# Kernel optimization log

Measured on AMD Instinct MI355X. Metric: run time of the kernel, lower is better.

The kernel has to match this reference:

```python
import jax, jax.numpy as jnp
import numpy as np

DIM = 1024
NUM_HEADS = 16
HEAD_DIM = DIM // NUM_HEADS
ROPE_BASE = 10000.0


def _rope_tables(seq_len, head_dim, dtype):
    # inv_freq over even indices, then freqs duplicated (cat(freqs, freqs))
    inv_freq = 1.0 / (ROPE_BASE ** (jnp.arange(0, head_dim, 2, dtype=jnp.float32) / head_dim))
    t = jnp.arange(seq_len, dtype=jnp.float32)
    freqs = jnp.einsum('i,j->ij', t, inv_freq)          # [N, head_dim/2]
    emb = jnp.concatenate([freqs, freqs], axis=-1)      # [N, head_dim]
    return jnp.cos(emb).astype(dtype), jnp.sin(emb).astype(dtype)


def _rotate_half(x):
    x1, x2 = jnp.split(x, 2, axis=-1)
    return jnp.concatenate([-x2, x1], axis=-1)


def setup_inputs() -> dict:
    key = jax.random.key(0)
    k1, k2, k3 = jax.random.split(key, 3)
    B, N = 2, 2048
    x = jax.random.normal(k1, (B, N, DIM), dtype=jnp.float32)
    w_qkv = jax.random.normal(k2, (3 * DIM, DIM), dtype=jnp.float32) * (DIM ** -0.5)
    w_out = jax.random.normal(k3, (DIM, DIM), dtype=jnp.float32) * (DIM ** -0.5)
    return {"x": x, "w_qkv": w_qkv, "w_out": w_out}


def reference(x, w_qkv, w_out):
    B, N, C = x.shape
    scale = HEAD_DIM ** -0.5
    qkv = x @ w_qkv.T                                   # [B, N, 3*C]
    qkv = qkv.reshape(B, N, 3, NUM_HEADS, HEAD_DIM)
    qkv = jnp.transpose(qkv, (2, 0, 3, 1, 4))           # [3, B, H, N, hd]
    q, k, v = qkv[0], qkv[1], qkv[2]

    cos, sin = _rope_tables(N, HEAD_DIM, x.dtype)       # [N, hd] each
    q = q * cos + _rotate_half(q) * sin
    k = k * cos + _rotate_half(k) * sin

    attn = jnp.einsum('bhqd,bhkd->bhqk', q, k) * scale  # [B, H, N, N]
    attn = jax.nn.softmax(attn, axis=-1)
    out = jnp.einsum('bhqk,bhkd->bhqd', attn, v)        # [B, H, N, hd]
    out = jnp.transpose(out, (0, 2, 1, 3)).reshape(B, N, C)
    return out @ w_out.T
```

## Files before the change

### kernel.cpp

```cpp
#include <hip/hip_runtime.h>
#include <stdint.h>


#define BATCH 2
#define SEQ   2048
#define DIM_C 1024
#define NHEAD 16
#define HD    64
#define MTOT  (BATCH * SEQ)
#define NQKV  (3 * DIM_C)
#define QSCALE 0.1803368801111204f

typedef _Float16 h8 __attribute__((ext_vector_type(8)));
typedef _Float16 h4v __attribute__((ext_vector_type(4)));
typedef float    f4 __attribute__((ext_vector_type(4)));

#if __has_builtin(__builtin_amdgcn_exp2f)
#define EXP2(x) __builtin_amdgcn_exp2f(x)
#else
#define EXP2(x) exp2f(x)
#endif

__device__ __forceinline__ f4 mfma16(h8 a, h8 b, f4 c) {
  return __builtin_amdgcn_mfma_f32_16x16x32_f16(a, b, c, 0, 0, 0);
}

__device__ __forceinline__ void gload16(const _Float16* g, _Float16* l) {
  __builtin_amdgcn_global_load_lds(
      (const __attribute__((address_space(1))) void*)g,
      (__attribute__((address_space(3))) void*)l, 16, 0, 0);
}

__global__ void cvt_kernel(const float* __restrict__ src, _Float16* __restrict__ dst, int n4) {
  int stride = gridDim.x * blockDim.x;
  for (int i = blockIdx.x * blockDim.x + threadIdx.x; i < n4; i += stride) {
    float4 v = reinterpret_cast<const float4*>(src)[i];
    h4v o = {(_Float16)v.x, (_Float16)v.y, (_Float16)v.z, (_Float16)v.w};
    reinterpret_cast<h4v*>(dst)[i] = o;
  }
}

__global__ void rope_table_kernel(float* __restrict__ cosT, float* __restrict__ sinT) {
  int idx = blockIdx.x * blockDim.x + threadIdx.x;
  int n = idx >> 5, j = idx & 31;
  float inv = powf(10000.0f, -(float)(2 * j) / 64.0f);
  float a = (float)n * inv;
  cosT[idx] = cosf(a);
  sinT[idx] = sinf(a);
}

template <int OUT_F16>
__global__ __launch_bounds__(256) void gemm_nt(const _Float16* __restrict__ A,
                                               const _Float16* __restrict__ Bm,
                                               void* __restrict__ Cv,
                                               int M, int N, int K) {
  __shared__ _Float16 Ah[2][128 * 32];
  __shared__ _Float16 Bh[2][128 * 32];
  const int tid = threadIdx.x;
  const int wave = tid >> 6, lane = tid & 63;
  const int lr = lane & 15, lg = lane >> 4;
  const int m0 = blockIdx.y * 128, n0 = blockIdx.x * 128;
  const int wr = (wave >> 1) * 64, wc = (wave & 1) * 64;

  const f4 zf = {0.f, 0.f, 0.f, 0.f};
  f4 acc[4][4];
#pragma unroll
  for (int i = 0; i < 4; ++i)
#pragma unroll
    for (int j = 0; j < 4; ++j) acc[i][j] = zf;

  const _Float16* Ab = A + (size_t)m0 * K;
  const _Float16* Bb = Bm + (size_t)n0 * K;

  auto stage = [&](int ks, int bi) {
#pragma unroll
    for (int it = 0; it < 2; ++it) {
      int c = tid + it * 256;
      int row = c >> 2, part = c & 3;
      gload16(Ab + (size_t)row * K + ks * 32 + part * 8, &Ah[bi][c * 8]);
      gload16(Bb + (size_t)row * K + ks * 32 + part * 8, &Bh[bi][c * 8]);
    }
  };

  stage(0, 0);
  const int ksteps = K >> 5;
  for (int ks = 0; ks < ksteps; ++ks) {
    __syncthreads();
    int cur = ks & 1;
    if (ks + 1 < ksteps) stage(ks + 1, cur ^ 1);

    h8 af[4], bf[4];
#pragma unroll
    for (int i = 0; i < 4; ++i) af[i] = *(const h8*)&Ah[cur][(wr + i * 16 + lr) * 32 + lg * 8];
#pragma unroll
    for (int j = 0; j < 4; ++j) bf[j] = *(const h8*)&Bh[cur][(wc + j * 16 + lr) * 32 + lg * 8];
#pragma unroll
    for (int i = 0; i < 4; ++i)
#pragma unroll
      for (int j = 0; j < 4; ++j) acc[i][j] = mfma16(af[i], bf[j], acc[i][j]);
  }

#pragma unroll
  for (int i = 0; i < 4; ++i)
#pragma unroll
    for (int j = 0; j < 4; ++j)
#pragma unroll
      for (int r = 0; r < 4; ++r) {
        size_t row = (size_t)(m0 + wr + i * 16 + lg * 4 + r);
        int col = n0 + wc + j * 16 + lr;
        if (OUT_F16)
          ((_Float16*)Cv)[row * N + col] = (_Float16)acc[i][j][r];
        else
          ((float*)Cv)[row * N + col] = acc[i][j][r];
      }
}

__global__ void rope_apply_kernel(const _Float16* __restrict__ qkv,
                                  const float* __restrict__ cosT,
                                  const float* __restrict__ sinT,
                                  _Float16* __restrict__ qh,
                                  _Float16* __restrict__ kh,
                                  _Float16* __restrict__ vh) {
  int idx = blockIdx.x * blockDim.x + threadIdx.x;
  int c8 = idx & 3;
  int t = idx >> 2;
  int h = t & 15;
  t >>= 4;
  int s = t % 3;
  int m = t / 3;
  int b = m >> 11, n = m & 2047;

  const _Float16* src = qkv + (size_t)m * NQKV + s * DIM_C + h * HD + c8 * 8;
  h8 x1 = *(const h8*)src;
  h8 x2 = *(const h8*)(src + 32);
  size_t o = ((size_t)((b * NHEAD + h) * SEQ + n)) * HD + c8 * 8;

  if (s == 2) {
    *(h8*)(vh + o) = x1;
    *(h8*)(vh + o + 32) = x2;
  } else {
    f4 cs0 = *(const f4*)(cosT + n * 32 + c8 * 8);
    f4 cs1 = *(const f4*)(cosT + n * 32 + c8 * 8 + 4);
    f4 sn0 = *(const f4*)(sinT + n * 32 + c8 * 8);
    f4 sn1 = *(const f4*)(sinT + n * 32 + c8 * 8 + 4);
    float scl = (s == 0) ? QSCALE : 1.0f;
    _Float16* dst = (s == 0) ? qh : kh;
    h8 o1, o2;
#pragma unroll
    for (int j = 0; j < 8; ++j) {
      float cv = (j < 4) ? cs0[j] : cs1[j - 4];
      float sv = (j < 4) ? sn0[j] : sn1[j - 4];
      float a1 = (float)x1[j], a2 = (float)x2[j];
      o1[j] = (_Float16)((a1 * cv - a2 * sv) * scl);
      o2[j] = (_Float16)((a2 * cv + a1 * sv) * scl);
    }
    *(h8*)(dst + o) = o1;
    *(h8*)(dst + o + 32) = o2;
  }
}

__global__ void vtrans_kernel(const _Float16* __restrict__ v, _Float16* __restrict__ vt) {
  int blk = blockIdx.x;
  int bh = blk >> 6, nt = blk & 63;
  int d = threadIdx.x & 63, w = threadIdx.x >> 6;
  int n0 = nt * 32 + w * 8;
  const _Float16* src = v + (size_t)bh * SEQ * HD;
  _Float16* dst = vt + ((size_t)bh * HD + d) * SEQ;
  h8 o;
#pragma unroll
  for (int j = 0; j < 8; ++j) o[j] = src[(size_t)(n0 + j) * HD + d];
  *(h8*)(dst + n0) = o;
}

__global__ __launch_bounds__(256) void attn_kernel(const _Float16* __restrict__ qh,
                                                   const _Float16* __restrict__ kh,
                                                   const _Float16* __restrict__ vt,
                                                   _Float16* __restrict__ aoh) {
  __shared__ _Float16 Kt[2][64 * 64];
  __shared__ _Float16 Vt[2][64 * 64];
  __shared__ _Float16 PlA[4][32][40], PlB[4][32][40];

  const int tid = threadIdx.x, wave = tid >> 6, lane = tid & 63;
  const int lr = lane & 15, lg = lane >> 4;
  const int bh = blockIdx.x >> 4;
  const int qt = blockIdx.x & 15;
  const int b = bh >> 4, h = bh & 15;

  const _Float16* Qb = qh + (size_t)bh * SEQ * HD;
  const _Float16* Kb = kh + (size_t)bh * SEQ * HD;
  const _Float16* Vb = vt + (size_t)bh * HD * SEQ;
  const int q0 = qt * 128 + wave * 32;

  const int cOf0 = ((lg) ^ (lr & 7)) * 8;
  const int cOf1 = ((4 + lg) ^ (lr & 7)) * 8;

  h8 aq[2][2];
#pragma unroll
  for (int r2 = 0; r2 < 2; ++r2)
#pragma unroll
    for (int c = 0; c < 2; ++c)
      aq[r2][c] = *(const h8*)(Qb + (size_t)(q0 + r2 * 16 + lr) * HD + c * 32 + lg * 8);

  float m_s[2] = {-1e30f, -1e30f}, l_s[2] = {0.f, 0.f};
  const f4 zf = {0.f, 0.f, 0.f, 0.f};
  f4 acc[2][4];
#pragma unroll
  for (int r2 = 0; r2 < 2; ++r2)
#pragma unroll
    for (int dt = 0; dt < 4; ++dt) acc[r2][dt] = zf;

  auto stage = [&](int kt, int bi) {
    const _Float16* Ks = Kb + (size_t)kt * 64 * HD;
    const _Float16* Vs = Vb + kt * 64;
#pragma unroll
    for (int it = 0; it < 2; ++it) {
      int c = tid + it * 256;
      int row = c >> 3, part = c & 7;
      int sp = part ^ (row & 7);
      gload16(Ks + (size_t)row * HD + sp * 8, &Kt[bi][c * 8]);
      gload16(Vs + (size_t)row * SEQ + sp * 8, &Vt[bi][c * 8]);
    }
  };

  stage(0, 0);
  for (int kt = 0; kt < SEQ / 64; ++kt) {
    __syncthreads();
    const int cur = kt & 1;
    if (kt + 1 < SEQ / 64) stage(kt + 1, cur ^ 1);

    const _Float16* Kbuf = &Kt[cur][0];
    const _Float16* Vbuf = &Vt[cur][0];
    h8 bk[4][2], vb[4][2];
#pragma unroll
    for (int ct = 0; ct < 4; ++ct) {
      bk[ct][0] = *(const h8*)(Kbuf + (ct * 16 + lr) * 64 + cOf0);
      bk[ct][1] = *(const h8*)(Kbuf + (ct * 16 + lr) * 64 + cOf1);
    }
#pragma unroll
    for (int dt = 0; dt < 4; ++dt) {
      vb[dt][0] = *(const h8*)(Vbuf + (dt * 16 + lr) * 64 + cOf0);
      vb[dt][1] = *(const h8*)(Vbuf + (dt * 16 + lr) * 64 + cOf1);
    }

#pragma unroll
    for (int r2 = 0; r2 < 2; ++r2) {
      f4 St[4];
      __builtin_amdgcn_s_setprio(1);
#pragma unroll
      for (int ct = 0; ct < 4; ++ct) {
        f4 z = mfma16(bk[ct][0], aq[r2][0], zf);
        St[ct] = mfma16(bk[ct][1], aq[r2][1], z);
      }
      __builtin_amdgcn_s_setprio(0);
      float pmax = fmaxf(fmaxf(fmaxf(St[0][0], St[0][1]), fmaxf(St[0][2], St[0][3])),
                         fmaxf(fmaxf(St[1][0], St[1][1]), fmaxf(St[1][2], St[1][3])));
      float pmax2 = fmaxf(fmaxf(fmaxf(St[2][0], St[2][1]), fmaxf(St[2][2], St[2][3])),
                          fmaxf(fmaxf(St[3][0], St[3][1]), fmaxf(St[3][2], St[3][3])));
      pmax = fmaxf(pmax, pmax2);
      pmax = fmaxf(pmax, __shfl_xor(pmax, 16));
      pmax = fmaxf(pmax, __shfl_xor(pmax, 32));

      bool grow = pmax > m_s[r2] + 8.f;
      if (__ballot(grow)) {
        float mn = fmaxf(m_s[r2], pmax);
        float al = EXP2(m_s[r2] - mn);
        m_s[r2] = mn;
        l_s[r2] *= al;
#pragma unroll
        for (int dt = 0; dt < 4; ++dt)
#pragma unroll
          for (int r = 0; r < 4; ++r) acc[r2][dt][r] *= al;
      }

      float rsum = 0.f;
#pragma unroll
      for (int ct = 0; ct < 4; ++ct)
#pragma unroll
        for (int r = 0; r < 4; ++r) {
          float p = EXP2(St[ct][r] - m_s[r2]);
          St[ct][r] = p;
          rsum += p;
        }
      rsum += __shfl_xor(rsum, 16);
      rsum += __shfl_xor(rsum, 32);
      l_s[r2] += rsum;

#pragma unroll
      for (int ct = 0; ct < 4; ++ct) {
        h4v pk = {(_Float16)St[ct][0], (_Float16)St[ct][1],
                  (_Float16)St[ct][2], (_Float16)St[ct][3]};
        if (ct < 2)
          *(h4v*)&PlA[wave][r2 * 16 + lr][ct * 16 + lg * 4] = pk;
        else
          *(h4v*)&PlB[wave][r2 * 16 + lr][(ct - 2) * 16 + lg * 4] = pk;
      }
    }

    __builtin_amdgcn_s_setprio(1);
#pragma unroll
    for (int r2 = 0; r2 < 2; ++r2)
#pragma unroll
      for (int c = 0; c < 2; ++c) {
        h8 pa = (c == 0) ? *(const h8*)&PlA[wave][r2 * 16 + lr][lg * 8]
                         : *(const h8*)&PlB[wave][r2 * 16 + lr][lg * 8];
#pragma unroll
        for (int dt = 0; dt < 4; ++dt)
          acc[r2][dt] = mfma16(vb[dt][c], pa, acc[r2][dt]);
      }
    __builtin_amdgcn_s_setprio(0);
  }

#pragma unroll
  for (int r2 = 0; r2 < 2; ++r2) {
    float inv = 1.0f / l_s[r2];
    int q = q0 + r2 * 16 + lr;
#pragma unroll
    for (int dt = 0; dt < 4; ++dt) {
      h4v o = {(_Float16)(acc[r2][dt][0] * inv), (_Float16)(acc[r2][dt][1] * inv),
               (_Float16)(acc[r2][dt][2] * inv), (_Float16)(acc[r2][dt][3] * inv)};
      *(h4v*)&aoh[((size_t)(b * SEQ + q)) * DIM_C + h * HD + dt * 16 + lg * 4] = o;
    }
  }
}

extern "C" void kernel_launch(void* const* d_in, const int* in_sizes, int n_in,
                              void* d_out, int out_size, void* d_ws, size_t ws_size,
                              hipStream_t stream) {
  const float* x     = (const float*)d_in[0];
  const float* w_qkv = (const float*)d_in[1];
  const float* w_out = (const float*)d_in[2];
  float* out = (float*)d_out;

  char* w = (char*)d_ws;
  _Float16* xh    = (_Float16*)(w + 0);
  _Float16* wqkvh = (_Float16*)(w + 8388608);
  _Float16* wouth = (_Float16*)(w + 14680064);
  _Float16* qkvh  = (_Float16*)(w + 16777216);
  _Float16* qhp   = (_Float16*)(w + 41943040);
  _Float16* khp   = (_Float16*)(w + 50331648);
  _Float16* vhp   = (_Float16*)(w + 58720256);
  _Float16* aohp  = (_Float16*)(w + 67108864);
  float*    cosT  = (float*)(w + 75497472);
  float*    sinT  = (float*)(w + 75759616);
  _Float16* vtp   = (_Float16*)(w + 16777216);

  cvt_kernel<<<1024, 256, 0, stream>>>(x, xh, MTOT * DIM_C / 4);
  cvt_kernel<<<1024, 256, 0, stream>>>(w_qkv, wqkvh, NQKV * DIM_C / 4);
  cvt_kernel<<<512, 256, 0, stream>>>(w_out, wouth, DIM_C * DIM_C / 4);
  rope_table_kernel<<<SEQ * 32 / 256, 256, 0, stream>>>(cosT, sinT);

  gemm_nt<1><<<dim3(NQKV / 128, MTOT / 128), 256, 0, stream>>>(
      xh, wqkvh, (void*)qkvh, MTOT, NQKV, DIM_C);

  rope_apply_kernel<<<MTOT * 3 * NHEAD * 4 / 256, 256, 0, stream>>>(
      qkvh, cosT, sinT, qhp, khp, vhp);

  vtrans_kernel<<<32 * 64, 256, 0, stream>>>(vhp, vtp);

  attn_kernel<<<32 * (SEQ / 128), 256, 0, stream>>>(qhp, khp, vtp, aohp);

  gemm_nt<0><<<dim3(DIM_C / 128, MTOT / 128), 256, 0, stream>>>(
      aohp, wouth, (void*)out, MTOT, DIM_C, DIM_C);
}
```

Baseline: 156.7 us.

## Fuse RoPE into QKV GEMM epilogue and restructure attention P handoff

Folds the RoPE application and head-major scatter into the QKV GEMM epilogue, which removes the separate rope_apply kernel and the intermediate QKV buffer round trip. The attention kernel now loads 128-key tiles instead of 64. It builds the P operand in registers using cvt_pkrtz plus permlane swaps rather than staging it through LDS, and computes the row sum with an MFMA against a ones vector. It also remaps block IDs for locality and sets launch bounds to 2 blocks per CU. The trade-offs are a larger LDS footprint, scattered 2-byte stores in the GEMM epilogue, and extra MFMA work for the row sums.

```diff
diff --git a/kernel.cpp b/kernel.cpp
--- a/kernel.cpp
+++ b/kernel.cpp
@@ -14,6 +14,7 @@
 typedef _Float16 h8 __attribute__((ext_vector_type(8)));
 typedef _Float16 h4v __attribute__((ext_vector_type(4)));
 typedef float    f4 __attribute__((ext_vector_type(4)));
+typedef unsigned int u4v __attribute__((ext_vector_type(4)));
 
 #if __has_builtin(__builtin_amdgcn_exp2f)
 #define EXP2(x) __builtin_amdgcn_exp2f(x)
@@ -23,6 +24,38 @@
 
 __device__ __forceinline__ f4 mfma16(h8 a, h8 b, f4 c) {
   return __builtin_amdgcn_mfma_f32_16x16x32_f16(a, b, c, 0, 0, 0);
+}
+
+__device__ __forceinline__ unsigned pk2(float a, float b) {
+  auto t = __builtin_amdgcn_cvt_pkrtz(a, b);
+  unsigned u;
+  __builtin_memcpy(&u, &t, 4);
+  return u;
+}
+
+__device__ __forceinline__ void swap32(unsigned& a, unsigned& b) {
+#if __has_builtin(__builtin_amdgcn_permlane32_swap)
+  typedef unsigned u2_ __attribute__((ext_vector_type(2)));
+  u2_ r = __builtin_amdgcn_permlane32_swap(a, b, false, false);
+  a = r[0]; b = r[1];
+#else
+  const bool hi = (threadIdx.x & 32) != 0;
+  unsigned sa = __shfl_xor(a, 32), sb = __shfl_xor(b, 32);
+  unsigned na = hi ? sb : a, nb = hi ? b : sa;
+  a = na; b = nb;
+#endif
+}
+__device__ __forceinline__ void swap16(unsigned& a, unsigned& b) {
+#if __has_builtin(__builtin_amdgcn_permlane16_swap)
+  typedef unsigned u2_ __attribute__((ext_vector_type(2)));
+  u2_ r = __builtin_amdgcn_permlane16_swap(a, b, false, false);
+  a = r[0]; b = r[1];
+#else
+  const bool hi = (threadIdx.x & 16) != 0;
+  unsigned sa = __shfl_xor(a, 16), sb = __shfl_xor(b, 16);
+  unsigned na = hi ? sb : a, nb = hi ? b : sa;
+  a = na; b = nb;
+#endif
 }
 
 __device__ __forceinline__ void gload16(const _Float16* g, _Float16* l) {
@@ -49,11 +82,14 @@
   sinT[idx] = sinf(a);
 }
 
-template <int OUT_F16>
-__global__ __launch_bounds__(256) void gemm_nt(const _Float16* __restrict__ A,
-                                               const _Float16* __restrict__ Bm,
-                                               void* __restrict__ Cv,
-                                               int M, int N, int K) {
+__global__ __launch_bounds__(256) void gemm_qkv(const _Float16* __restrict__ A,
+                                                const _Float16* __restrict__ Bm,
+                                                const float* __restrict__ cosT,
+                                                const float* __restrict__ sinT,
+                                                _Float16* __restrict__ qh,
+                                                _Float16* __restrict__ kh,
+                                                _Float16* __restrict__ vh) {
+  const int K = DIM_C;
   __shared__ _Float16 Ah[2][128 * 32];
   __shared__ _Float16 Bh[2][128 * 32];
   const int tid = threadIdx.x;
@@ -100,6 +136,86 @@
       for (int j = 0; j < 4; ++j) acc[i][j] = mfma16(af[i], bf[j], acc[i][j]);
   }
 
+  const int nc = n0 + wc;
+  const int s = nc >> 10;
+  const int hcol = (nc >> 6) & 15;
+  _Float16* dst = (s == 0) ? qh : (s == 1) ? kh : vh;
+  const float scl = (s == 0) ? QSCALE : 1.0f;
+#pragma unroll
+  for (int i = 0; i < 4; ++i)
+#pragma unroll
+    for (int r = 0; r < 4; ++r) {
+      int row = m0 + wr + i * 16 + lg * 4 + r;
+      int n = row & (SEQ - 1);
+      _Float16* drow = dst + ((size_t)(((row >> 11) * NHEAD + hcol) * SEQ + n)) * HD;
+      if (s == 2) {
+        drow[lr]      = (_Float16)acc[i][0][r];
+        drow[lr + 16] = (_Float16)acc[i][1][r];
+        drow[lr + 32] = (_Float16)acc[i][2][r];
+        drow[lr + 48] = (_Float16)acc[i][3][r];
+      } else {
+        float c0 = cosT[n * 32 + lr],      sn0 = sinT[n * 32 + lr];
+        float c1 = cosT[n * 32 + 16 + lr], sn1 = sinT[n * 32 + 16 + lr];
+        float a10 = acc[i][0][r], a20 = acc[i][2][r];
+        float a11 = acc[i][1][r], a21 = acc[i][3][r];
+        drow[lr]      = (_Float16)((a10 * c0 - a20 * sn0) * scl);
+        drow[lr + 32] = (_Float16)((a20 * c0 + a10 * sn0) * scl);
+        drow[lr + 16] = (_Float16)((a11 * c1 - a21 * sn1) * scl);
+        drow[lr + 48] = (_Float16)((a21 * c1 + a11 * sn1) * scl);
+      }
+    }
+}
+
+__global__ __launch_bounds__(256) void gemm_out(const _Float16* __restrict__ A,
+                                                const _Float16* __restrict__ Bm,
+                                                float* __restrict__ Cv,
+                                                int M, int N, int K) {
+  __shared__ _Float16 Ah[2][128 * 32];
+  __shared__ _Float16 Bh[2][128 * 32];
+  const int tid = threadIdx.x;
+  const int wave = tid >> 6, lane = tid & 63;
+  const int lr = lane & 15, lg = lane >> 4;
+  const int m0 = blockIdx.y * 128, n0 = blockIdx.x * 128;
+  const int wr = (wave >> 1) * 64, wc = (wave & 1) * 64;
+
+  const f4 zf = {0.f, 0.f, 0.f, 0.f};
+  f4 acc[4][4];
+#pragma unroll
+  for (int i = 0; i < 4; ++i)
+#pragma unroll
+    for (int j = 0; j < 4; ++j) acc[i][j] = zf;
+
+  const _Float16* Ab = A + (size_t)m0 * K;
+  const _Float16* Bb = Bm + (size_t)n0 * K;
+
+  auto stage = [&](int ks, int bi) {
+#pragma unroll
+    for (int it = 0; it < 2; ++it) {
+      int c = tid + it * 256;
+      int row = c >> 2, part = c & 3;
+      gload16(Ab + (size_t)row * K + ks * 32 + part * 8, &Ah[bi][c * 8]);
+      gload16(Bb + (size_t)row * K + ks * 32 + part * 8, &Bh[bi][c * 8]);
+    }
+  };
+
+  stage(0, 0);
+  const int ksteps = K >> 5;
+  for (int ks = 0; ks < ksteps; ++ks) {
+    __syncthreads();
+    int cur = ks & 1;
+    if (ks + 1 < ksteps) stage(ks + 1, cur ^ 1);
+
+    h8 af[4], bf[4];
+#pragma unroll
+    for (int i = 0; i < 4; ++i) af[i] = *(const h8*)&Ah[cur][(wr + i * 16 + lr) * 32 + lg * 8];
+#pragma unroll
+    for (int j = 0; j < 4; ++j) bf[j] = *(const h8*)&Bh[cur][(wc + j * 16 + lr) * 32 + lg * 8];
+#pragma unroll
+    for (int i = 0; i < 4; ++i)
+#pragma unroll
+      for (int j = 0; j < 4; ++j) acc[i][j] = mfma16(af[i], bf[j], acc[i][j]);
+  }
+
 #pragma unroll
   for (int i = 0; i < 4; ++i)
 #pragma unroll
@@ -108,55 +224,8 @@
       for (int r = 0; r < 4; ++r) {
         size_t row = (size_t)(m0 + wr + i * 16 + lg * 4 + r);
         int col = n0 + wc + j * 16 + lr;
-        if (OUT_F16)
-          ((_Float16*)Cv)[row * N + col] = (_Float16)acc[i][j][r];
-        else
-          ((float*)Cv)[row * N + col] = acc[i][j][r];
+        Cv[row * N + col] = acc[i][j][r];
       }
-}
-
-__global__ void rope_apply_kernel(const _Float16* __restrict__ qkv,
-                                  const float* __restrict__ cosT,
-                                  const float* __restrict__ sinT,
-                                  _Float16* __restrict__ qh,
-                                  _Float16* __restrict__ kh,
-                                  _Float16* __restrict__ vh) {
-  int idx = blockIdx.x * blockDim.x + threadIdx.x;
-  int c8 = idx & 3;
-  int t = idx >> 2;
-  int h = t & 15;
-  t >>= 4;
-  int s = t % 3;
-  int m = t / 3;
-  int b = m >> 11, n = m & 2047;
-
-  const _Float16* src = qkv + (size_t)m * NQKV + s * DIM_C + h * HD + c8 * 8;
-  h8 x1 = *(const h8*)src;
-  h8 x2 = *(const h8*)(src + 32);
-  size_t o = ((size_t)((b * NHEAD + h) * SEQ + n)) * HD + c8 * 8;
-
-  if (s == 2) {
-    *(h8*)(vh + o) = x1;
-    *(h8*)(vh + o + 32) = x2;
-  } else {
-    f4 cs0 = *(const f4*)(cosT + n * 32 + c8 * 8);
-    f4 cs1 = *(const f4*)(cosT + n * 32 + c8 * 8 + 4);
-    f4 sn0 = *(const f4*)(sinT + n * 32 + c8 * 8);
-    f4 sn1 = *(const f4*)(sinT + n * 32 + c8 * 8 + 4);
-    float scl = (s == 0) ? QSCALE : 1.0f;
-    _Float16* dst = (s == 0) ? qh : kh;
-    h8 o1, o2;
-#pragma unroll
-    for (int j = 0; j < 8; ++j) {
-      float cv = (j < 4) ? cs0[j] : cs1[j - 4];
-      float sv = (j < 4) ? sn0[j] : sn1[j - 4];
-      float a1 = (float)x1[j], a2 = (float)x2[j];
-      o1[j] = (_Float16)((a1 * cv - a2 * sv) * scl);
-      o2[j] = (_Float16)((a2 * cv + a1 * sv) * scl);
-    }
-    *(h8*)(dst + o) = o1;
-    *(h8*)(dst + o + 32) = o2;
-  }
 }
 
 __global__ void vtrans_kernel(const _Float16* __restrict__ v, _Float16* __restrict__ vt) {
@@ -172,18 +241,19 @@
   *(h8*)(dst + n0) = o;
 }
 
-__global__ __launch_bounds__(256) void attn_kernel(const _Float16* __restrict__ qh,
-                                                   const _Float16* __restrict__ kh,
-                                                   const _Float16* __restrict__ vt,
-                                                   _Float16* __restrict__ aoh) {
-  __shared__ _Float16 Kt[2][64 * 64];
-  __shared__ _Float16 Vt[2][64 * 64];
-  __shared__ _Float16 PlA[4][32][40], PlB[4][32][40];
+__global__ __launch_bounds__(256, 2) void attn_kernel(const _Float16* __restrict__ qh,
+                                                      const _Float16* __restrict__ kh,
+                                                      const _Float16* __restrict__ vt,
+                                                      _Float16* __restrict__ aoh) {
+  __shared__ _Float16 Kt[2][128 * 64];
+  __shared__ _Float16 Vt[2][64 * 128];
 
   const int tid = threadIdx.x, wave = tid >> 6, lane = tid & 63;
   const int lr = lane & 15, lg = lane >> 4;
-  const int bh = blockIdx.x >> 4;
-  const int qt = blockIdx.x & 15;
+  const int p = blockIdx.x;
+  const int wg = (p & 7) * 64 + (p >> 3);
+  const int bh = wg >> 4;
+  const int qt = wg & 15;
   const int b = bh >> 4, h = bh & 15;
 
   const _Float16* Qb = qh + (size_t)bh * SEQ * HD;
@@ -191,8 +261,13 @@
   const _Float16* Vb = vt + (size_t)bh * HD * SEQ;
   const int q0 = qt * 128 + wave * 32;
 
-  const int cOf0 = ((lg) ^ (lr & 7)) * 8;
-  const int cOf1 = ((4 + lg) ^ (lr & 7)) * 8;
+  int kOf[2], vOf[2][2];
+#pragma unroll
+  for (int cc = 0; cc < 2; ++cc) kOf[cc] = ((cc * 4 + lg) ^ (lr & 7)) * 8;
+#pragma unroll
+  for (int sub = 0; sub < 2; ++sub)
+#pragma unroll
+    for (int cc = 0; cc < 2; ++cc) vOf[sub][cc] = ((sub * 8 + cc * 4 + lg) ^ lr) * 8;
 
   h8 aq[2][2];
 #pragma unroll
@@ -201,8 +276,11 @@
     for (int c = 0; c < 2; ++c)
       aq[r2][c] = *(const h8*)(Qb + (size_t)(q0 + r2 * 16 + lr) * HD + c * 32 + lg * 8);
 
-  float m_s[2] = {-1e30f, -1e30f}, l_s[2] = {0.f, 0.f};
+  const h8 onesv = {(_Float16)1.f, (_Float16)1.f, (_Float16)1.f, (_Float16)1.f,
+                    (_Float16)1.f, (_Float16)1.f, (_Float16)1.f, (_Float16)1.f};
+  float m_s[2] = {-1e30f, -1e30f};
   const f4 zf = {0.f, 0.f, 0.f, 0.f};
+  f4 lacc[2] = {zf, zf};
   f4 acc[2][4];
 #pragma unroll
   for (int r2 = 0; r2 < 2; ++r2)
@@ -210,109 +288,107 @@
     for (int dt = 0; dt < 4; ++dt) acc[r2][dt] = zf;
 
   auto stage = [&](int kt, int bi) {
-    const _Float16* Ks = Kb + (size_t)kt * 64 * HD;
-    const _Float16* Vs = Vb + kt * 64;
-#pragma unroll
-    for (int it = 0; it < 2; ++it) {
+    const _Float16* Ks = Kb + (size_t)kt * 128 * HD;
+    const _Float16* Vs = Vb + kt * 128;
+#pragma unroll
+    for (int it = 0; it < 4; ++it) {
       int c = tid + it * 256;
-      int row = c >> 3, part = c & 7;
-      int sp = part ^ (row & 7);
-      gload16(Ks + (size_t)row * HD + sp * 8, &Kt[bi][c * 8]);
-      gload16(Vs + (size_t)row * SEQ + sp * 8, &Vt[bi][c * 8]);
+      int krow = c >> 3, kpart = c & 7;
+      int ksp = kpart ^ (krow & 7);
+      gload16(Ks + (size_t)krow * HD + ksp * 8, &Kt[bi][c * 8]);
+      int vrow = c >> 4, vpart = c & 15;
+      int vsp = vpart ^ (vrow & 15);
+      gload16(Vs + (size_t)vrow * SEQ + vsp * 8, &Vt[bi][c * 8]);
     }
   };
 
   stage(0, 0);
-  for (int kt = 0; kt < SEQ / 64; ++kt) {
+  for (int t = 0; t < SEQ / 128; ++t) {
     __syncthreads();
-    const int cur = kt & 1;
-    if (kt + 1 < SEQ / 64) stage(kt + 1, cur ^ 1);
+    const int cur = t & 1;
+    if (t + 1 < SEQ / 128) stage(t + 1, cur ^ 1);
 
     const _Float16* Kbuf = &Kt[cur][0];
     const _Float16* Vbuf = &Vt[cur][0];
-    h8 bk[4][2], vb[4][2];
-#pragma unroll
-    for (int ct = 0; ct < 4; ++ct) {
-      bk[ct][0] = *(const h8*)(Kbuf + (ct * 16 + lr) * 64 + cOf0);
-      bk[ct][1] = *(const h8*)(Kbuf + (ct * 16 + lr) * 64 + cOf1);
-    }
-#pragma unroll
-    for (int dt = 0; dt < 4; ++dt) {
-      vb[dt][0] = *(const h8*)(Vbuf + (dt * 16 + lr) * 64 + cOf0);
-      vb[dt][1] = *(const h8*)(Vbuf + (dt * 16 + lr) * 64 + cOf1);
-    }
-
-#pragma unroll
-    for (int r2 = 0; r2 < 2; ++r2) {
-      f4 St[4];
-      __builtin_amdgcn_s_setprio(1);
-#pragma unroll
-      for (int ct = 0; ct < 4; ++ct) {
-        f4 z = mfma16(bk[ct][0], aq[r2][0], zf);
-        St[ct] = mfma16(bk[ct][1], aq[r2][1], z);
+#pragma unroll
+    for (int sub = 0; sub < 2; ++sub) {
+      h8 bk[4][2], vb[4][2];
+      const _Float16* Krow = Kbuf + (sub * 64 + lr) * 64;
+#pragma unroll
+      for (int ct = 0; ct < 4; ++ct)
+#pragma unroll
+        for (int cc = 0; cc < 2; ++cc)
+          bk[ct][cc] = *(const h8*)(Krow + ct * 16 * 64 + kOf[cc]);
+      const _Float16* Vrow = Vbuf + lr * 128;
+#pragma unroll
+      for (int dt = 0; dt < 4; ++dt)
+#pragma unroll
+        for (int cc = 0; cc < 2; ++cc)
+          vb[dt][cc] = *(const h8*)(Vrow + dt * 16 * 128 + vOf[sub][cc]);
+
+#pragma unroll
+      for (int r2 = 0; r2 < 2; ++r2) {
+        f4 St[4];
+        __builtin_amdgcn_s_setprio(1);
+#pragma unroll
+        for (int ct = 0; ct < 4; ++ct) {
+          f4 z = mfma16(bk[ct][0], aq[r2][0], zf);
+          St[ct] = mfma16(bk[ct][1], aq[r2][1], z);
+        }
+        __builtin_amdgcn_s_setprio(0);
+        float pmax = fmaxf(fmaxf(fmaxf(St[0][0], St[0][1]), fmaxf(St[0][2], St[0][3])),
+                           fmaxf(fmaxf(St[1][0], St[1][1]), fmaxf(St[1][2], St[1][3])));
+        float pmax2 = fmaxf(fmaxf(fmaxf(St[2][0], St[2][1]), fmaxf(St[2][2], St[2][3])),
+                            fmaxf(fmaxf(St[3][0], St[3][1]), fmaxf(St[3][2], St[3][3])));
+        pmax = fmaxf(pmax, pmax2);
+        pmax = fmaxf(pmax, __shfl_xor(pmax, 16));
+        pmax = fmaxf(pmax, __shfl_xor(pmax, 32));
+
+        bool grow = pmax > m_s[r2] + 8.f;
+        if (__ballot(grow)) {
+          float mn = fmaxf(m_s[r2], pmax);
+          float al = EXP2(m_s[r2] - mn);
+          m_s[r2] = mn;
+          lacc[r2] *= al;
+#pragma unroll
+          for (int dt = 0; dt < 4; ++dt)
+#pragma unroll
+            for (int r = 0; r < 4; ++r) acc[r2][dt][r] *= al;
+        }
+
+        const float m = m_s[r2];
+        unsigned w[4][2];
+#pragma unroll
+        for (int ct = 0; ct < 4; ++ct) {
+          w[ct][0] = pk2(EXP2(St[ct][0] - m), EXP2(St[ct][1] - m));
+          w[ct][1] = pk2(EXP2(St[ct][2] - m), EXP2(St[ct][3] - m));
+        }
+        swap32(w[0][0], w[1][0]); swap32(w[0][1], w[1][1]);
+        swap32(w[2][0], w[3][0]); swap32(w[2][1], w[3][1]);
+        swap16(w[0][0], w[1][0]); swap16(w[0][1], w[1][1]);
+        swap16(w[2][0], w[3][0]); swap16(w[2][1], w[3][1]);
+        u4v pw0 = {w[0][0], w[0][1], w[1][0], w[1][1]};
+        u4v pw1 = {w[2][0], w[2][1], w[3][0], w[3][1]};
+        h8 pa0, pa1;
+        __builtin_memcpy(&pa0, &pw0, 16);
+        __builtin_memcpy(&pa1, &pw1, 16);
+
+        __builtin_amdgcn_s_setprio(1);
+        lacc[r2] = mfma16(onesv, pa0, lacc[r2]);
+        lacc[r2] = mfma16(onesv, pa1, lacc[r2]);
+#pragma unroll
+        for (int dt = 0; dt < 4; ++dt) {
+          acc[r2][dt] = mfma16(vb[dt][0], pa0, acc[r2][dt]);
+          acc[r2][dt] = mfma16(vb[dt][1], pa1, acc[r2][dt]);
+        }
+        __builtin_amdgcn_s_setprio(0);
       }
-      __builtin_amdgcn_s_setprio(0);
-      float pmax = fmaxf(fmaxf(fmaxf(St[0][0], St[0][1]), fmaxf(St[0][2], St[0][3])),
-                         fmaxf(fmaxf(St[1][0], St[1][1]), fmaxf(St[1][2], St[1][3])));
-      float pmax2 = fmaxf(fmaxf(fmaxf(St[2][0], St[2][1]), fmaxf(St[2][2], St[2][3])),
-                          fmaxf(fmaxf(St[3][0], St[3][1]), fmaxf(St[3][2], St[3][3])));
-      pmax = fmaxf(pmax, pmax2);
-      pmax = fmaxf(pmax, __shfl_xor(pmax, 16));
-      pmax = fmaxf(pmax, __shfl_xor(pmax, 32));
-
-      bool grow = pmax > m_s[r2] + 8.f;
-      if (__ballot(grow)) {
-        float mn = fmaxf(m_s[r2], pmax);
-        float al = EXP2(m_s[r2] - mn);
-        m_s[r2] = mn;
-        l_s[r2] *= al;
-#pragma unroll
-        for (int dt = 0; dt < 4; ++dt)
-#pragma unroll
-          for (int r = 0; r < 4; ++r) acc[r2][dt][r] *= al;
-      }
-
-      float rsum = 0.f;
-#pragma unroll
-      for (int ct = 0; ct < 4; ++ct)
-#pragma unroll
-        for (int r = 0; r < 4; ++r) {
-          float p = EXP2(St[ct][r] - m_s[r2]);
-          St[ct][r] = p;
-          rsum += p;
-        }
-      rsum += __shfl_xor(rsum, 16);
-      rsum += __shfl_xor(rsum, 32);
-      l_s[r2] += rsum;
-
-#pragma unroll
-      for (int ct = 0; ct < 4; ++ct) {
-        h4v pk = {(_Float16)St[ct][0], (_Float16)St[ct][1],
-                  (_Float16)St[ct][2], (_Float16)St[ct][3]};
-        if (ct < 2)
-          *(h4v*)&PlA[wave][r2 * 16 + lr][ct * 16 + lg * 4] = pk;
-        else
-          *(h4v*)&PlB[wave][r2 * 16 + lr][(ct - 2) * 16 + lg * 4] = pk;
-      }
-    }
-
-    __builtin_amdgcn_s_setprio(1);
-#pragma unroll
-    for (int r2 = 0; r2 < 2; ++r2)
-#pragma unroll
-      for (int c = 0; c < 2; ++c) {
-        h8 pa = (c == 0) ? *(const h8*)&PlA[wave][r2 * 16 + lr][lg * 8]
-                         : *(const h8*)&PlB[wave][r2 * 16 + lr][lg * 8];
-#pragma unroll
-        for (int dt = 0; dt < 4; ++dt)
-          acc[r2][dt] = mfma16(vb[dt][c], pa, acc[r2][dt]);
-      }
-    __builtin_amdgcn_s_setprio(0);
+    }
   }
 
 #pragma unroll
   for (int r2 = 0; r2 < 2; ++r2) {
-    float inv = 1.0f / l_s[r2];
+    float inv = 1.0f / lacc[r2][0];
     int q = q0 + r2 * 16 + lr;
 #pragma unroll
     for (int dt = 0; dt < 4; ++dt) {
@@ -335,30 +411,26 @@
   _Float16* xh    = (_Float16*)(w + 0);
   _Float16* wqkvh = (_Float16*)(w + 8388608);
   _Float16* wouth = (_Float16*)(w + 14680064);
-  _Float16* qkvh  = (_Float16*)(w + 16777216);
-  _Float16* qhp   = (_Float16*)(w + 41943040);
-  _Float16* khp   = (_Float16*)(w + 50331648);
-  _Float16* vhp   = (_Float16*)(w + 58720256);
-  _Float16* aohp  = (_Float16*)(w + 67108864);
-  float*    cosT  = (float*)(w + 75497472);
-  float*    sinT  = (float*)(w + 75759616);
-  _Float16* vtp   = (_Float16*)(w + 16777216);
+  _Float16* qhp   = (_Float16*)(w + 16777216);
+  _Float16* khp   = (_Float16*)(w + 25165824);
+  _Float16* vhp   = (_Float16*)(w + 33554432);
+  _Float16* vtp   = (_Float16*)(w + 41943040);
+  _Float16* aohp  = (_Float16*)(w + 50331648);
+  float*    cosT  = (float*)(w + 58720256);
+  float*    sinT  = (float*)(w + 58982400);
 
   cvt_kernel<<<1024, 256, 0, stream>>>(x, xh, MTOT * DIM_C / 4);
   cvt_kernel<<<1024, 256, 0, stream>>>(w_qkv, wqkvh, NQKV * DIM_C / 4);
   cvt_kernel<<<512, 256, 0, stream>>>(w_out, wouth, DIM_C * DIM_C / 4);
   rope_table_kernel<<<SEQ * 32 / 256, 256, 0, stream>>>(cosT, sinT);
 
-  gemm_nt<1><<<dim3(NQKV / 128, MTOT / 128), 256, 0, stream>>>(
-      xh, wqkvh, (void*)qkvh, MTOT, NQKV, DIM_C);
-
-  rope_apply_kernel<<<MTOT * 3 * NHEAD * 4 / 256, 256, 0, stream>>>(
-      qkvh, cosT, sinT, qhp, khp, vhp);
+  gemm_qkv<<<dim3(NQKV / 128, MTOT / 128), 256, 0, stream>>>(
+      xh, wqkvh, cosT, sinT, qhp, khp, vhp);
 
   vtrans_kernel<<<32 * 64, 256, 0, stream>>>(vhp, vtp);
 
-  attn_kernel<<<32 * (SEQ / 128), 256, 0, stream>>>(qhp, khp, vtp, aohp);
-
-  gemm_nt<0><<<dim3(DIM_C / 128, MTOT / 128), 256, 0, stream>>>(
-      aohp, wouth, (void*)out, MTOT, DIM_C, DIM_C);
-}
+  attn_kernel<<<32 * 16, 256, 0, stream>>>(qhp, khp, vtp, aohp);
+
+  gemm_out<<<dim3(DIM_C / 128, MTOT / 128), 256, 0, stream>>>(
+      aohp, wouth, out, MTOT, DIM_C, DIM_C);
+}
```

After: 142.8 us. 8.9% less time.
